# Performance work log

Measured on AMD Instinct MI355X. Metric: run time of the kernel, lower is better.

The kernel has to match this reference:

```python
import jax, jax.numpy as jnp
import numpy as np
from jax import lax

B = 16384; T = 4; DY = 2; H = 64; K = 4; DIM = T * DY
LR = 0.1; EPS_GOAL = 1.0; B1 = 0.9; B2 = 0.999; ADAM_EPS = 1e-8
LOG2PI = float(np.log(2.0 * np.pi))


def setup_inputs() -> dict:
    key = jax.random.key(0)
    ks = jax.random.split(key, 16)
    r = lambda i, shape, s=1.0: jax.random.normal(ks[i], shape, dtype=jnp.float32) * s
    return {
        "visual_features": r(0, (B, 128)),
        "velocity": r(1, (B, 3)),
        "is_at_traffic_light": jax.random.uniform(ks[2], (B, 1), dtype=jnp.float32),
        "traffic_light_state": jax.random.uniform(ks[3], (B, 1), dtype=jnp.float32),
        "goal": r(4, (B, K, DY), 2.0),
        "base_sample": r(5, (DIM,)),
        # merger MLP: 133 -> 64 -> 64 -> 64, ReLU incl. final
        "Wm1": r(6, (133, H), 0.08), "bm1": jnp.zeros((H,), jnp.float32),
        "Wm2": r(7, (H, H), 0.12), "bm2": jnp.zeros((H,), jnp.float32),
        "Wm3": r(8, (H, H), 0.12), "bm3": jnp.zeros((H,), jnp.float32),
        # GRUCell(input=2, hidden=64), torch layout [3H, in], [3H, H]
        "w_ih": r(9, (3 * H, DY), 0.12), "w_hh": r(10, (3 * H, H), 0.12),
        "b_ih": jnp.zeros((3 * H,), jnp.float32), "b_hh": jnp.zeros((3 * H,), jnp.float32),
        # locscale MLP: 64 -> 32 (ReLU) -> 4
        "Wl1": r(11, (H, 32), 0.12), "bl1": jnp.zeros((32,), jnp.float32),
        "Wl2": r(12, (32, 4), 0.12), "bl2": jnp.zeros((4,), jnp.float32),
        "num_steps": 8,
    }


def _gru(x, h, w_ih, w_hh, b_ih, b_hh):
    gi = x @ w_ih.T + b_ih
    gh = h @ w_hh.T + b_hh
    ir, iz, in_ = jnp.split(gi, 3, axis=-1)
    hr, hz, hn = jnp.split(gh, 3, axis=-1)
    r = jax.nn.sigmoid(ir + hr)
    u = jax.nn.sigmoid(iz + hz)
    n = jnp.tanh(in_ + r * hn)
    return (1.0 - u) * n + u * h


def _step_params(y_tm1, z, p):
    w_ih, w_hh, b_ih, b_hh, Wl1, bl1, Wl2, bl2 = p
    z = _gru(y_tm1, z, w_ih, w_hh, b_ih, b_hh)
    ls = jax.nn.relu(z @ Wl1 + bl1) @ Wl2 + bl2  # [B,4]
    dloc = ls[..., :2]
    scale = jax.nn.softplus(ls[..., 2:]) + 0.001
    return z, dloc, scale


def _flow_forward(x, z0, p):
    Bsz = x.shape[0]
    def step(carry, x_t):
        y_tm1, z = carry
        z, dloc, scale = _step_params(y_tm1, z, p)
        y_t = y_tm1 + dloc + scale * x_t
        return (y_t, z), (y_t, scale)
    _, (ys, scales) = lax.scan(step, (jnp.zeros((Bsz, DY), x.dtype), z0), jnp.swapaxes(x, 0, 1))
    y = jnp.swapaxes(ys, 0, 1)        # [B,T,2]
    scales = jnp.swapaxes(scales, 0, 1)
    logabsdet = jnp.sum(jnp.log(jnp.abs(jnp.prod(scales, axis=1))), axis=-1)  # [B]
    return y, logabsdet


def _flow_inverse(y, z0, p):
    Bsz = y.shape[0]
    def step(carry, y_t):
        y_tm1, z = carry
        z, dloc, scale = _step_params(y_tm1, z, p)
        x_t = (y_t - (y_tm1 + dloc)) / scale
        return (y_t, z), (x_t, scale)
    _, (xs, scales) = lax.scan(step, (jnp.zeros((Bsz, DY), y.dtype), z0), jnp.swapaxes(y, 0, 1))
    x = jnp.swapaxes(xs, 0, 1)        # [B,T,2]
    scales = jnp.swapaxes(scales, 0, 1)
    xf = x.reshape(Bsz, -1)
    log_prob = -0.5 * jnp.sum(xf * xf, axis=-1) - 0.5 * DIM * LOG2PI  # std MVN, identity cov
    logabsdet = jnp.sum(jnp.log(jnp.abs(jnp.prod(scales, axis=-1))), axis=-1)  # [B]
    return x, log_prob, logabsdet


def _goal_likelihood(y, goal):
    yl = y[:, -1, :]                               # [B,2]
    d = (yl[:, None, :] - goal) / EPS_GOAL         # [B,K,2]
    comp = -0.5 * jnp.sum(d * d, axis=-1) - DY * (float(np.log(EPS_GOAL)) + 0.5 * LOG2PI)
    lp = jax.nn.logsumexp(comp, axis=-1) - float(np.log(K))
    return jnp.mean(lp)


def _model_forward(visual_features, velocity, is_at_traffic_light, traffic_light_state,
                   goal, base_sample, Wm1, bm1, Wm2, bm2, Wm3, bm3,
                   w_ih, w_hh, b_ih, b_hh, Wl1, bl1, Wl2, bl2, num_steps):
    p = (w_ih, w_hh, b_ih, b_hh, Wl1, bl1, Wl2, bl2)
    feats = jnp.concatenate([visual_features, velocity, is_at_traffic_light, traffic_light_state], axis=-1)
    z = jax.nn.relu(feats @ Wm1 + bm1)
    z = jax.nn.relu(z @ Wm2 + bm2)
    z = jax.nn.relu(z @ Wm3 + bm3)                 # [B,64] contextual params
    Bsz = visual_features.shape[0]
    x0 = jnp.tile(base_sample[None, :], (Bsz, 1)).reshape(Bsz, T, DY)

    def loss_fn(x):
        y, _ = _flow_forward(x, z, p)
        _, log_prob, logabsdet = _flow_inverse(y, z, p)
        imitation_prior = jnp.mean(log_prob - logabsdet)
        return -(imitation_prior + _goal_likelihood(y, goal))

    vg = jax.value_and_grad(loss_fn)

    def adam_step(carry, t):
        x, m, v, xb, lb = carry
        loss, g = vg(x)
        m = B1 * m + (1.0 - B1) * g
        v = B2 * v + (1.0 - B2) * (g * g)
        mh = m / (1.0 - B1 ** t)
        vh = v / (1.0 - B2 ** t)
        xn = x - LR * mh / (jnp.sqrt(vh) + ADAM_EPS)
        better = loss < lb  # torch keeps post-step x when pre-step loss improves
        xb = jnp.where(better, xn, xb)
        lb = jnp.where(better, loss, lb)
        return (xn, m, v, xb, lb), None

    ts = jnp.arange(1, int(num_steps) + 1, dtype=jnp.float32)
    (_, _, _, x_best, _), _ = lax.scan(
        adam_step, (x0, jnp.zeros_like(x0), jnp.zeros_like(x0), x0, jnp.float32(1000.0)), ts)
    y, _ = _flow_forward(x_best, z, p)
    return y


def reference(visual_features, velocity, is_at_traffic_light, traffic_light_state,
              goal, base_sample, Wm1, bm1, Wm2, bm2, Wm3, bm3,
              w_ih, w_hh, b_ih, b_hh, Wl1, bl1, Wl2, bl2, num_steps):
    return _model_forward(visual_features, velocity, is_at_traffic_light, traffic_light_state,
                          goal, base_sample, Wm1, bm1, Wm2, bm2, Wm3, bm3,
                          w_ih, w_hh, b_ih, b_hh, Wl1, bl1, Wl2, bl2, num_steps)
```

## Files before the change

### kernel.cpp

```cpp
#include <hip/hip_runtime.h>
#include <math.h>

#define BATCH 16384
#define NSMAX 8
#define LOG2PI_F 1.8378770664093453f
#define LOG4_F 1.3862943611198906f

typedef _Float16 v8h __attribute__((ext_vector_type(8)));
typedef float    v4f __attribute__((ext_vector_type(4)));
typedef float    v2f __attribute__((ext_vector_type(2)));

#define MFMA16(A,B,C) __builtin_amdgcn_mfma_f32_16x16x32_f16(A,B,C,0,0,0)

__device__ __forceinline__ float bcast(float v, int l) {
    return __uint_as_float(__builtin_amdgcn_readlane(__float_as_uint(v), (unsigned)l));
}
__device__ __forceinline__ float fsigm(float v){ return 1.f/(1.f + __expf(-v)); }
__device__ __forceinline__ float ftanh(float v){ return 1.f - 2.f/(__expf(2.f*v)+1.f); }
__device__ __forceinline__ float fsp(float v){ return fmaxf(v,0.f) + __logf(1.f + __expf(-fabsf(v))); }

__device__ __forceinline__ v8h ld8(const float* p){
    v4f a = *(const v4f*)p; v4f b = *(const v4f*)(p+4);
    v8h r;
    r[0]=(_Float16)a[0]; r[1]=(_Float16)a[1]; r[2]=(_Float16)a[2]; r[3]=(_Float16)a[3];
    r[4]=(_Float16)b[0]; r[5]=(_Float16)b[1]; r[6]=(_Float16)b[2]; r[7]=(_Float16)b[3];
    return r;
}
__device__ __forceinline__ v8h ld8lo(const float* p){
    v4f a = *(const v4f*)p; v4f b = *(const v4f*)(p+4);
    v8h r;
    #pragma unroll
    for (int j=0;j<4;++j){ _Float16 h=(_Float16)a[j]; r[j]=(_Float16)(a[j]-(float)h); }
    #pragma unroll
    for (int j=0;j<4;++j){ _Float16 h=(_Float16)b[j]; r[4+j]=(_Float16)(b[j]-(float)h); }
    return r;
}
__device__ __forceinline__ v8h ld8s(const float* p, int stride){
    v8h r;
    #pragma unroll
    for (int j=0;j<8;++j) r[j] = (_Float16)p[j*stride];
    return r;
}
__device__ __forceinline__ v8h ld8slo(const float* p, int stride){
    v8h r;
    #pragma unroll
    for (int j=0;j<8;++j){ float v=p[j*stride]; _Float16 h=(_Float16)v; r[j]=(_Float16)(v-(float)h); }
    return r;
}
__device__ __forceinline__ unsigned packh2(float a, float b){
    unsigned short au = __builtin_bit_cast(unsigned short, (_Float16)a);
    unsigned short bu = __builtin_bit_cast(unsigned short, (_Float16)b);
    return (unsigned)au | ((unsigned)bu<<16);
}
__device__ __forceinline__ float unpk_lo(unsigned p){
    return (float)__builtin_bit_cast(_Float16,(unsigned short)(p&0xffff));
}
__device__ __forceinline__ float unpk_hi(unsigned p){
    return (float)__builtin_bit_cast(_Float16,(unsigned short)(p>>16));
}

__global__ __launch_bounds__(512) void k_mlp(
    const float* __restrict__ visual, const float* __restrict__ vel,
    const float* __restrict__ tl, const float* __restrict__ tls,
    const float* __restrict__ Wm1, const float* __restrict__ bm1,
    const float* __restrict__ Wm2, const float* __restrict__ bm2,
    const float* __restrict__ Wm3, const float* __restrict__ bm3,
    float* __restrict__ z0ws)
{
    __shared__ float smem[9600];
    const int tid  = threadIdx.x;
    const int lane = tid & 63;
    const int w    = tid >> 6;
    const int b    = blockIdx.x * 8 + w;
    for (int i = tid; i < 8512; i += 512) smem[i] = Wm1[i];
    float* sfeat = smem + 8512 + w * 136;
    sfeat[lane]      = visual[b*128 + lane];
    sfeat[64 + lane] = visual[b*128 + 64 + lane];
    if (lane < 3)  sfeat[128 + lane] = vel[b*3 + lane];
    if (lane == 3) sfeat[131] = tl[b];
    if (lane == 4) sfeat[132] = tls[b];
    __syncthreads();
    float acc = bm1[lane];
    for (int f = 0; f < 133; ++f) acc = fmaf(smem[f*64 + lane], sfeat[f], acc);
    float z1 = fmaxf(acc, 0.f);
    __syncthreads();
    for (int i = tid; i < 4096; i += 512) smem[i] = Wm2[i];
    __syncthreads();
    acc = bm2[lane];
    #pragma unroll 8
    for (int kk = 0; kk < 64; ++kk) acc = fmaf(smem[kk*64 + lane], bcast(z1, kk), acc);
    float z2 = fmaxf(acc, 0.f);
    __syncthreads();
    for (int i = tid; i < 4096; i += 512) smem[i] = Wm3[i];
    __syncthreads();
    acc = bm3[lane];
    #pragma unroll 8
    for (int kk = 0; kk < 64; ++kk) acc = fmaf(smem[kk*64 + lane], bcast(z2, kk), acc);
    z0ws[(size_t)b*64 + lane] = fmaxf(acc, 0.f);
}

__global__ __launch_bounds__(128, 1) void k_adam(
    const float* __restrict__ goal, const float* __restrict__ bs,
    const float* __restrict__ wih, const float* __restrict__ whh,
    const float* __restrict__ bih, const float* __restrict__ bhh,
    const float* __restrict__ Wl1, const float* __restrict__ bl1,
    const float* __restrict__ Wl2, const float* __restrict__ bl2,
    const int*  __restrict__ nsp, const float* __restrict__ z0ws,
    float* __restrict__ traj, float* __restrict__ parts,
    _Float16* __restrict__ ckpt)
{
    __shared__ _Float16 gruLo[12288];
    __shared__ _Float16 whhTf[12288];
    __shared__ _Float16 stageL[2][3200];
    __shared__ float    xsx[2][256];

    const int tid  = threadIdx.x;
    const int w    = tid >> 6;
    const int ln   = tid & 63;
    const int col  = ln & 15;
    const int quad = ln >> 4;
    const int b0   = blockIdx.x*32 + w*16;
    _Float16* sw = stageL[w];
    float*    xw = xsx[w];

    for (int i = tid; i < 24*64; i += 128){
        int f = i>>6, l = i&63, lc = l&15, lq = l>>4;
        int T = f>>1, K = f&1;
        v8h lo = ld8lo(whh + (lc+16*T)*64 + 32*K + lq*8);
        *(v8h*)(gruLo + f*512 + l*8) = lo;
        int Tz = f/6, kc = f - Tz*6;
        v8h th = ld8s(whh + (kc*32+lq*8)*64 + lc + 16*Tz, 64);
        *(v8h*)(whhTf + f*512 + l*8) = th;
    }
    __syncthreads();

    v8h bwh[12][2];
    #pragma unroll
    for (int T=0;T<12;++T){
        int c = col + 16*T;
        bwh[T][0] = ld8(whh + c*64 +      quad*8);
        bwh[T][1] = ld8(whh + c*64 + 32 + quad*8);
    }
    v8h w1h[2][2], w1l[2][2];
    #pragma unroll
    for (int T=0;T<2;++T){
        int n = col + 16*T;
        w1h[T][0] = ld8s  (Wl1 + (     quad*8)*32 + n, 32);
        w1h[T][1] = ld8s  (Wl1 + (32 + quad*8)*32 + n, 32);
        w1l[T][0] = ld8slo(Wl1 + (     quad*8)*32 + n, 32);
        w1l[T][1] = ld8slo(Wl1 + (32 + quad*8)*32 + n, 32);
    }
    v8h awl1[4];
    #pragma unroll
    for (int Tz=0;Tz<4;++Tz)
        awl1[Tz] = ld8(Wl1 + (col+16*Tz)*32 + quad*8);

    float wi0[12], wi1[12];
    #pragma unroll
    for (int T=0;T<12;++T){
        int c = col + 16*T;
        wi0[T] = wih[c*2]; wi1[T] = wih[c*2+1];
    }
    float bsum[8], bn_i[4], bn_h[4];
    #pragma unroll
    for (int T=0;T<8;++T) bsum[T] = bih[col+16*T] + bhh[col+16*T];
    #pragma unroll
    for (int T=0;T<4;++T){
        bn_i[T] = bih[128+col+16*T];
        bn_h[T] = bhh[128+col+16*T];
    }
    float w2[2][4], bl1v[2];
    #pragma unroll
    for (int T=0;T<2;++T){
        int i5 = col + 16*T;
        bl1v[T] = bl1[i5];
        #pragma unroll
        for (int j=0;j<4;++j) w2[T][j] = Wl2[i5*4+j];
    }
    float b2[4] = {bl2[0], bl2[1], bl2[2], bl2[3]};

    float xa0 = bs[2*quad], xa1 = bs[2*quad+1];
    xw[col*16 + 2*quad]   = xa0;
    xw[col*16 + 2*quad+1] = xa1;
    float am0=0,am1=0,av0=0,av1=0,pb1=1.f,pb2=1.f;

    int ns = *nsp; if (ns > NSMAX) ns = NSMAX;

    unsigned rnp[4][4];
    float ug[4][4], ghs[4][4], aa[2][4];
    float s0v[4], s1v[4], c0v[4], c1v[4];
    float zc[4][4];

    auto cell = [&](bool split, const float (&yp0)[4], const float (&yp1)[4],
                    const float (&zprev)[4][4]){
        v8h ah0 = *(const v8h*)(sw + col*200 +      quad*8);
        v8h ah1 = *(const v8h*)(sw + col*200 + 32 + quad*8);
        v8h al0, al1;
        if (split){
            al0 = *(const v8h*)(sw + col*200 + 64 + quad*8);
            al1 = *(const v8h*)(sw + col*200 + 96 + quad*8);
        }
        float znew[4][4];
        #pragma unroll
        for (int Tz=0;Tz<4;++Tz){
            int tr = Tz, tu = Tz+4, tn = Tz+8;
            v8h lr0 = *(const v8h*)(gruLo + (tr*2  )*512 + ln*8);
            v8h lr1 = *(const v8h*)(gruLo + (tr*2+1)*512 + ln*8);
            v8h lu0 = *(const v8h*)(gruLo + (tu*2  )*512 + ln*8);
            v8h lu1 = *(const v8h*)(gruLo + (tu*2+1)*512 + ln*8);
            v8h ln0 = *(const v8h*)(gruLo + (tn*2  )*512 + ln*8);
            v8h ln1 = *(const v8h*)(gruLo + (tn*2+1)*512 + ln*8);
            v4f gr = {0,0,0,0}, gu = {0,0,0,0}, gn = {0,0,0,0};
            gr = MFMA16(ah0, lr0, gr);   gr = MFMA16(ah1, lr1, gr);
            gu = MFMA16(ah0, lu0, gu);   gu = MFMA16(ah1, lu1, gu);
            gn = MFMA16(ah0, ln0, gn);   gn = MFMA16(ah1, ln1, gn);
            if (split){
                gr = MFMA16(al0, bwh[tr][0], gr); gr = MFMA16(al1, bwh[tr][1], gr);
                gu = MFMA16(al0, bwh[tu][0], gu); gu = MFMA16(al1, bwh[tu][1], gu);
                gn = MFMA16(al0, bwh[tn][0], gn); gn = MFMA16(al1, bwh[tn][1], gn);
            }
            gr = MFMA16(ah0, bwh[tr][0], gr); gr = MFMA16(ah1, bwh[tr][1], gr);
            gu = MFMA16(ah0, bwh[tu][0], gu); gu = MFMA16(ah1, bwh[tu][1], gu);
            gn = MFMA16(ah0, bwh[tn][0], gn); gn = MFMA16(ah1, bwh[tn][1], gn);
            #pragma unroll
            for (int r=0;r<4;++r){
                float pr = gr[r] + wi0[Tz]*yp0[r]   + wi1[Tz]*yp1[r]   + bsum[Tz];
                float pu = gu[r] + wi0[Tz+4]*yp0[r] + wi1[Tz+4]*yp1[r] + bsum[Tz+4];
                float gh = gn[r] + bn_h[Tz];
                float gi = wi0[Tz+8]*yp0[r] + wi1[Tz+8]*yp1[r] + bn_i[Tz];
                float R = fsigm(pr), U = fsigm(pu);
                float N = ftanh(gi + R*gh);
                if (!split){ rnp[Tz][r]=packh2(R,N); ug[Tz][r]=U; ghs[Tz][r]=gh; }
                znew[Tz][r] = (1.f-U)*N + U*zprev[Tz][r];
            }
        }
        if (split){
            #pragma unroll
            for (int Tz=0;Tz<4;++Tz)
                #pragma unroll
                for (int r=0;r<4;++r){
                    float v = znew[Tz][r];
                    zc[Tz][r] = v;
                    _Float16 h = (_Float16)v;
                    int o = (quad*4+r)*200 + col + 16*Tz;
                    sw[o] = h; sw[o+64] = (_Float16)(v-(float)h);
                }
        } else {
            #pragma unroll
            for (int Tz=0;Tz<4;++Tz)
                #pragma unroll
                for (int r=0;r<4;++r)
                    sw[(quad*4+r)*200 + col + 16*Tz] = (_Float16)znew[Tz][r];
        }
        v8h bh0 = *(const v8h*)(sw + col*200 +      quad*8);
        v8h bh1 = *(const v8h*)(sw + col*200 + 32 + quad*8);
        v8h bl0, blf;
        if (split){
            bl0 = *(const v8h*)(sw + col*200 + 64 + quad*8);
            blf = *(const v8h*)(sw + col*200 + 96 + quad*8);
        }
        #pragma unroll
        for (int T=0;T<2;++T){
            v4f acc = {0.f,0.f,0.f,0.f};
            acc = MFMA16(bh0, w1l[T][0], acc);
            acc = MFMA16(bh1, w1l[T][1], acc);
            if (split){
                acc = MFMA16(bl0, w1h[T][0], acc);
                acc = MFMA16(blf, w1h[T][1], acc);
            }
            acc = MFMA16(bh0, w1h[T][0], acc);
            acc = MFMA16(bh1, w1h[T][1], acc);
            #pragma unroll
            for (int r=0;r<4;++r) aa[T][r] = fmaxf(acc[r] + bl1v[T], 0.f);
        }
        #pragma unroll
        for (int r=0;r<4;++r){
            float q2 = aa[0][r]*w2[0][2] + aa[1][r]*w2[1][2];
            float q3 = aa[0][r]*w2[0][3] + aa[1][r]*w2[1][3];
            float q0 = 0.f, q1 = 0.f;
            if (split){
                q0 = aa[0][r]*w2[0][0] + aa[1][r]*w2[1][0];
                q1 = aa[0][r]*w2[0][1] + aa[1][r]*w2[1][1];
            }
            #pragma unroll
            for (int m=1;m<16;m<<=1){
                q2 += __shfl_xor(q2,m); q3 += __shfl_xor(q3,m);
                if (split){ q0 += __shfl_xor(q0,m); q1 += __shfl_xor(q1,m); }
            }
            if (split){ c0v[r] = q0 + b2[0]; c1v[r] = q1 + b2[1]; }
            s0v[r] = fsp(q2 + b2[2]) + 0.001f;
            s1v[r] = fsp(q3 + b2[3]) + 0.001f;
        }
    };

    const int crow = ln >> 2;
    const int ccol = (ln & 3) * 16;

    for (int s=0; s<ns; ++s){
        #pragma unroll
        for (int Tz=0;Tz<4;++Tz)
            #pragma unroll
            for (int r=0;r<4;++r){
                float v = z0ws[(size_t)(b0+quad*4+r)*64 + col + 16*Tz];
                zc[Tz][r] = v;
                _Float16 h = (_Float16)v;
                int o = (quad*4+r)*200 + col + 16*Tz;
                sw[o] = h; sw[o+64] = (_Float16)(v-(float)h);
            }
        float y0[4]={0,0,0,0}, y1[4]={0,0,0,0};
        float sumls[4]={0,0,0,0}, sumx2[4]={0,0,0,0};
        #pragma unroll
        for (int t=0;t<4;++t){
            float zprev[4][4];
            #pragma unroll
            for (int Tz=0;Tz<4;++Tz)
                #pragma unroll
                for (int r=0;r<4;++r) zprev[Tz][r] = zc[Tz][r];
            cell(true, y0, y1, zprev);
            #pragma unroll
            for (int r=0;r<4;++r){
                v2f xv = *(const v2f*)(&xw[(quad*4+r)*16 + 2*t]);
                sumx2[r] += xv[0]*xv[0] + xv[1]*xv[1];
                y0[r] += c0v[r] + s0v[r]*xv[0];
                y1[r] += c1v[r] + s1v[r]*xv[1];
                int o = (quad*4+r)*200 + 192 + 2*t;
                sw[o] = (_Float16)y0[r]; sw[o+1] = (_Float16)y1[r];
                sumls[r] += __logf(s0v[r]) + __logf(s1v[r]);
            }
            if (t<3){
                v8h z1 = *(const v8h*)(sw + crow*200 + ccol);
                v8h z2 = *(const v8h*)(sw + crow*200 + ccol + 8);
                _Float16* gp = ckpt + ((size_t)t*BATCH + (b0+crow))*64 + ccol;
                *(v8h*)gp = z1; *(v8h*)(gp+8) = z2;
            }
        }
        float cel[4], yb0[4], yb1[4];
        #pragma unroll
        for (int r=0;r<4;++r){
            const float* gpt = goal + (size_t)(b0+quad*4+r)*8;
            v4f ga = *(const v4f*)gpt; v4f gb = *(const v4f*)(gpt+4);
            float c0_ = -0.5f*((y0[r]-ga[0])*(y0[r]-ga[0]) + (y1[r]-ga[1])*(y1[r]-ga[1])) - LOG2PI_F;
            float c1_ = -0.5f*((y0[r]-ga[2])*(y0[r]-ga[2]) + (y1[r]-ga[3])*(y1[r]-ga[3])) - LOG2PI_F;
            float c2_ = -0.5f*((y0[r]-gb[0])*(y0[r]-gb[0]) + (y1[r]-gb[1])*(y1[r]-gb[1])) - LOG2PI_F;
            float c3_ = -0.5f*((y0[r]-gb[2])*(y0[r]-gb[2]) + (y1[r]-gb[3])*(y1[r]-gb[3])) - LOG2PI_F;
            float mx = fmaxf(fmaxf(c0_,c1_), fmaxf(c2_,c3_));
            float e0 = __expf(c0_-mx), e1 = __expf(c1_-mx), e2 = __expf(c2_-mx), e3 = __expf(c3_-mx);
            float se = e0+e1+e2+e3;
            float lp = mx + __logf(se) - LOG4_F;
            cel[r] = -0.5f*sumx2[r] - 4.f*LOG2PI_F - sumls[r] + lp;
            float inv = 1.f/se;
            yb0[r] = inv*(e0*(ga[0]-y0[r]) + e1*(ga[2]-y0[r]) + e2*(gb[0]-y0[r]) + e3*(gb[2]-y0[r]));
            yb1[r] = inv*(e0*(ga[1]-y1[r]) + e1*(ga[3]-y1[r]) + e2*(gb[1]-y1[r]) + e3*(gb[3]-y1[r]));
        }
        float tsum = cel[0]+cel[1]+cel[2]+cel[3];
        tsum += __shfl_xor(tsum,16); tsum += __shfl_xor(tsum,32);
        if (ln==0) parts[s*1024 + blockIdx.x*2 + w] = tsum;

        float zbN[4][4];
        #pragma unroll
        for (int Tz=0;Tz<4;++Tz){ zbN[Tz][0]=0;zbN[Tz][1]=0;zbN[Tz][2]=0;zbN[Tz][3]=0; }
        #pragma unroll
        for (int tt=0; tt<4; ++tt){
            const int t = 3-tt;
            float zcp[4][4];
            if (t > 0){
                const _Float16* gp = ckpt + ((size_t)(t-1)*BATCH + (b0+crow))*64 + ccol;
                v8h z1 = *(const v8h*)gp; v8h z2 = *(const v8h*)(gp+8);
                *(v8h*)(sw + crow*200 + ccol) = z1;
                *(v8h*)(sw + crow*200 + ccol + 8) = z2;
                #pragma unroll
                for (int Tz=0;Tz<4;++Tz)
                    #pragma unroll
                    for (int r=0;r<4;++r)
                        zcp[Tz][r] = (float)sw[(quad*4+r)*200 + col + 16*Tz];
            } else {
                #pragma unroll
                for (int Tz=0;Tz<4;++Tz)
                    #pragma unroll
                    for (int r=0;r<4;++r){
                        _Float16 h = (_Float16)z0ws[(size_t)(b0+quad*4+r)*64 + col + 16*Tz];
                        zcp[Tz][r] = (float)h;
                        sw[(quad*4+r)*200 + col + 16*Tz] = h;
                    }
            }
            float yp0[4], yp1[4];
            #pragma unroll
            for (int r=0;r<4;++r){
                if (t==0){ yp0[r]=0.f; yp1[r]=0.f; }
                else {
                    int o = (quad*4+r)*200 + 192 + 2*(t-1);
                    yp0[r] = (float)sw[o]; yp1[r] = (float)sw[o+1];
                }
            }
            cell(false, yp0, yp1, zcp);

            float l2[4], l3[4];
            #pragma unroll
            for (int r=0;r<4;++r){
                v2f xv = *(const v2f*)(&xw[(quad*4+r)*16 + 2*t]);
                float sb0 = yb0[r]*xv[0] - 1.f/s0v[r];
                float sb1 = yb1[r]*xv[1] - 1.f/s1v[r];
                float sg0 = 1.f - __expf(-(s0v[r]-0.001f));
                float sg1 = 1.f - __expf(-(s1v[r]-0.001f));
                l2[r] = sb0*sg0; l3[r] = sb1*sg1;
                v2f xb; xb[0] = yb0[r]*s0v[r] - xv[0]; xb[1] = yb1[r]*s1v[r] - xv[1];
                *(v2f*)(&xw[(quad*4+r)*16 + 8 + 2*t]) = xb;
            }
            #pragma unroll
            for (int T=0;T<2;++T)
                #pragma unroll
                for (int r=0;r<4;++r){
                    float ab = w2[T][0]*yb0[r] + w2[T][1]*yb1[r] + w2[T][2]*l2[r] + w2[T][3]*l3[r];
                    ab = (aa[T][r] > 0.f) ? ab : 0.f;
                    sw[(quad*4+r)*200 + 128 + col + 16*T] = (_Float16)ab;
                }
            v8h a_ab = *(const v8h*)(sw + col*200 + 128 + quad*8);
            float dzt[4][4];
            #pragma unroll
            for (int Tz=0;Tz<4;++Tz){
                v4f acc = { zbN[Tz][0], zbN[Tz][1], zbN[Tz][2], zbN[Tz][3] };
                acc = MFMA16(a_ab, awl1[Tz], acc);
                #pragma unroll
                for (int r=0;r<4;++r) dzt[Tz][r] = acc[r];
            }
            float px0[4] = {0,0,0,0}, px1[4] = {0,0,0,0};
            #pragma unroll
            for (int Tz=0;Tz<4;++Tz)
                #pragma unroll
                for (int r=0;r<4;++r){
                    float R = unpk_lo(rnp[Tz][r]);
                    float N = unpk_hi(rnp[Tz][r]);
                    float U = ug[Tz][r], GH = ghs[Tz][r];
                    float nb = dzt[Tz][r]*(1.f-U);
                    float dn = nb*(1.f-N*N);
                    float gnb = dn*R;
                    float rb  = dn*GH;
                    float dr  = rb*R*(1.f-R);
                    float du  = dzt[Tz][r]*(zcp[Tz][r]-N)*U*(1.f-U);
                    int o = (quad*4+r)*200 + col + 16*Tz;
                    sw[o]       = (_Float16)dr;
                    sw[o + 64]  = (_Float16)du;
                    sw[o + 128] = (_Float16)gnb;
                    px0[r] += dr*wi0[Tz] + du*wi0[Tz+4] + dn*wi0[Tz+8];
                    px1[r] += dr*wi1[Tz] + du*wi1[Tz+4] + dn*wi1[Tz+8];
                }
            v8h adg[6];
            #pragma unroll
            for (int kc=0;kc<6;++kc)
                adg[kc] = *(const v8h*)(sw + col*200 + kc*32 + quad*8);
            #pragma unroll
            for (int Tz=0;Tz<4;++Tz){
                v4f acc = { dzt[Tz][0]*ug[Tz][0], dzt[Tz][1]*ug[Tz][1],
                            dzt[Tz][2]*ug[Tz][2], dzt[Tz][3]*ug[Tz][3] };
                #pragma unroll
                for (int kc=0;kc<6;++kc){
                    v8h bwt = *(const v8h*)(whhTf + (Tz*6+kc)*512 + ln*8);
                    acc = MFMA16(adg[kc], bwt, acc);
                }
                #pragma unroll
                for (int r=0;r<4;++r) zbN[Tz][r] = acc[r];
            }
            #pragma unroll
            for (int r=0;r<4;++r){
                float p0 = px0[r], p1 = px1[r];
                #pragma unroll
                for (int m=1;m<16;m<<=1){ p0 += __shfl_xor(p0,m); p1 += __shfl_xor(p1,m); }
                yb0[r] += p0; yb1[r] += p1;
            }
        }
        v2f xb = *(const v2f*)(&xw[col*16 + 8 + 2*quad]);
        float g0 = xb[0] * (-1.f/16384.f), g1 = xb[1] * (-1.f/16384.f);
        am0 = 0.9f*am0 + 0.1f*g0;        am1 = 0.9f*am1 + 0.1f*g1;
        av0 = 0.999f*av0 + 0.001f*g0*g0; av1 = 0.999f*av1 + 0.001f*g1*g1;
        pb1 *= 0.9f; pb2 *= 0.999f;
        float ic1 = 1.f/(1.f-pb1), ic2 = 1.f/(1.f-pb2);
        xa0 -= 0.1f*(am0*ic1)/(sqrtf(av0*ic2) + 1e-8f);
        xa1 -= 0.1f*(am1*ic1)/(sqrtf(av1*ic2) + 1e-8f);
        xw[col*16 + 2*quad]   = xa0;
        xw[col*16 + 2*quad+1] = xa1;
        v2f tv; tv[0]=xa0; tv[1]=xa1;
        *(v2f*)(traj + (size_t)(b0+col)*64 + s*8 + 2*quad) = tv;
    }
}

__global__ void k_pick(const int* __restrict__ nsp,
                       const float* __restrict__ parts, int* __restrict__ best)
{
    int ln = threadIdx.x & 63;
    int ns = *nsp; if (ns > NSMAX) ns = NSMAX;
    float losses[NSMAX];
    for (int s=0;s<NSMAX;++s){
        float acc = 0.f;
        if (s < ns){
            for (int i=ln;i<1024;i+=64) acc += parts[s*1024+i];
            #pragma unroll
            for (int m=1;m<64;m<<=1) acc += __shfl_xor(acc,m);
        }
        losses[s] = -acc * (1.f/16384.f);
    }
    if (ln==0 && blockIdx.x==0){
        float lb = 1000.f; int bi = -1;
        for (int s=0;s<ns;++s) if (losses[s] < lb){ lb = losses[s]; bi = s; }
        best[0] = bi;
    }
}

__global__ __launch_bounds__(128, 1) void k_final(
    const float* __restrict__ bs,
    const float* __restrict__ wih, const float* __restrict__ whh,
    const float* __restrict__ bih, const float* __restrict__ bhh,
    const float* __restrict__ Wl1, const float* __restrict__ bl1,
    const float* __restrict__ Wl2, const float* __restrict__ bl2,
    const float* __restrict__ z0ws, const float* __restrict__ traj,
    const int* __restrict__ best, float* __restrict__ outp)
{
    __shared__ _Float16 gruLo[12288];
    __shared__ _Float16 stageL[2][3200];
    __shared__ float    xsx[2][128];

    const int tid  = threadIdx.x;
    const int w    = tid >> 6;
    const int ln   = tid & 63;
    const int col  = ln & 15;
    const int quad = ln >> 4;
    const int b0   = blockIdx.x*32 + w*16;
    _Float16* sw = stageL[w];
    float*    xw = xsx[w];

    for (int i = tid; i < 24*64; i += 128){
        int f = i>>6, l = i&63, lc = l&15, lq = l>>4;
        int T = f>>1, K = f&1;
        v8h lo = ld8lo(whh + (lc+16*T)*64 + 32*K + lq*8);
        *(v8h*)(gruLo + f*512 + l*8) = lo;
    }
    __syncthreads();

    v8h bwh[12][2];
    #pragma unroll
    for (int T=0;T<12;++T){
        int c = col + 16*T;
        bwh[T][0] = ld8(whh + c*64 +      quad*8);
        bwh[T][1] = ld8(whh + c*64 + 32 + quad*8);
    }
    v8h w1h[2][2], w1l[2][2];
    #pragma unroll
    for (int T=0;T<2;++T){
        int n = col + 16*T;
        w1h[T][0] = ld8s  (Wl1 + (     quad*8)*32 + n, 32);
        w1h[T][1] = ld8s  (Wl1 + (32 + quad*8)*32 + n, 32);
        w1l[T][0] = ld8slo(Wl1 + (     quad*8)*32 + n, 32);
        w1l[T][1] = ld8slo(Wl1 + (32 + quad*8)*32 + n, 32);
    }
    float wi0[12], wi1[12], bsum[8], bn_i[4], bn_h[4];
    #pragma unroll
    for (int T=0;T<12;++T){
        int c = col + 16*T;
        wi0[T] = wih[c*2]; wi1[T] = wih[c*2+1];
    }
    #pragma unroll
    for (int T=0;T<8;++T) bsum[T] = bih[col+16*T] + bhh[col+16*T];
    #pragma unroll
    for (int T=0;T<4;++T){
        bn_i[T] = bih[128+col+16*T];
        bn_h[T] = bhh[128+col+16*T];
    }
    float w2[2][4], bl1v[2];
    #pragma unroll
    for (int T=0;T<2;++T){
        int i5 = col + 16*T;
        bl1v[T] = bl1[i5];
        #pragma unroll
        for (int j=0;j<4;++j) w2[T][j] = Wl2[i5*4+j];
    }
    float b2[4] = {bl2[0], bl2[1], bl2[2], bl2[3]};

    float zc[4][4];
    #pragma unroll
    for (int Tz=0;Tz<4;++Tz)
        #pragma unroll
        for (int r=0;r<4;++r){
            float v = z0ws[(size_t)(b0+quad*4+r)*64 + col + 16*Tz];
            zc[Tz][r] = v;
            _Float16 h = (_Float16)v;
            int o = (quad*4+r)*200 + col + 16*Tz;
            sw[o] = h; sw[o+64] = (_Float16)(v-(float)h);
        }

    int bi = best[0];
    float x0i, x1i;
    if (bi >= 0){
        v2f xv = *(const v2f*)(traj + (size_t)(b0+col)*64 + bi*8 + 2*quad);
        x0i = xv[0]; x1i = xv[1];
    } else { x0i = bs[2*quad]; x1i = bs[2*quad+1]; }
    xw[col*8 + 2*quad]   = x0i;
    xw[col*8 + 2*quad+1] = x1i;

    float y0[4]={0,0,0,0}, y1[4]={0,0,0,0};
    #pragma unroll
    for (int t=0;t<4;++t){
        v8h ah0 = *(const v8h*)(sw + col*200 +      quad*8);
        v8h ah1 = *(const v8h*)(sw + col*200 + 32 + quad*8);
        v8h al0 = *(const v8h*)(sw + col*200 + 64 + quad*8);
        v8h al1 = *(const v8h*)(sw + col*200 + 96 + quad*8);
        #pragma unroll
        for (int Tz=0;Tz<4;++Tz){
            int tr = Tz, tu = Tz+4, tn = Tz+8;
            v8h lr0 = *(const v8h*)(gruLo + (tr*2  )*512 + ln*8);
            v8h lr1 = *(const v8h*)(gruLo + (tr*2+1)*512 + ln*8);
            v8h lu0 = *(const v8h*)(gruLo + (tu*2  )*512 + ln*8);
            v8h lu1 = *(const v8h*)(gruLo + (tu*2+1)*512 + ln*8);
            v8h ln0 = *(const v8h*)(gruLo + (tn*2  )*512 + ln*8);
            v8h ln1 = *(const v8h*)(gruLo + (tn*2+1)*512 + ln*8);
            v4f gr = {0,0,0,0}, gu = {0,0,0,0}, gn = {0,0,0,0};
            gr = MFMA16(ah0, lr0, gr);   gr = MFMA16(ah1, lr1, gr);
            gu = MFMA16(ah0, lu0, gu);   gu = MFMA16(ah1, lu1, gu);
            gn = MFMA16(ah0, ln0, gn);   gn = MFMA16(ah1, ln1, gn);
            gr = MFMA16(al0, bwh[tr][0], gr); gr = MFMA16(al1, bwh[tr][1], gr);
            gu = MFMA16(al0, bwh[tu][0], gu); gu = MFMA16(al1, bwh[tu][1], gu);
            gn = MFMA16(al0, bwh[tn][0], gn); gn = MFMA16(al1, bwh[tn][1], gn);
            gr = MFMA16(ah0, bwh[tr][0], gr); gr = MFMA16(ah1, bwh[tr][1], gr);
            gu = MFMA16(ah0, bwh[tu][0], gu); gu = MFMA16(ah1, bwh[tu][1], gu);
            gn = MFMA16(ah0, bwh[tn][0], gn); gn = MFMA16(ah1, bwh[tn][1], gn);
            #pragma unroll
            for (int r=0;r<4;++r){
                float pr = gr[r] + wi0[Tz]*y0[r]   + wi1[Tz]*y1[r]   + bsum[Tz];
                float pu = gu[r] + wi0[Tz+4]*y0[r] + wi1[Tz+4]*y1[r] + bsum[Tz+4];
                float gh = gn[r] + bn_h[Tz];
                float gi = wi0[Tz+8]*y0[r] + wi1[Tz+8]*y1[r] + bn_i[Tz];
                float R = fsigm(pr), U = fsigm(pu);
                float N = ftanh(gi + R*gh);
                zc[Tz][r] = (1.f-U)*N + U*zc[Tz][r];
            }
        }
        #pragma unroll
        for (int Tz=0;Tz<4;++Tz)
            #pragma unroll
            for (int r=0;r<4;++r){
                float v = zc[Tz][r];
                _Float16 h = (_Float16)v;
                int o = (quad*4+r)*200 + col + 16*Tz;
                sw[o] = h; sw[o+64] = (_Float16)(v-(float)h);
            }
        v8h bh0 = *(const v8h*)(sw + col*200 +      quad*8);
        v8h bh1 = *(const v8h*)(sw + col*200 + 32 + quad*8);
        v8h bl0 = *(const v8h*)(sw + col*200 + 64 + quad*8);
        v8h blf = *(const v8h*)(sw + col*200 + 96 + quad*8);
        float aaf[2][4];
        #pragma unroll
        for (int T=0;T<2;++T){
            v4f acc = {0.f,0.f,0.f,0.f};
            acc = MFMA16(bh0, w1l[T][0], acc);
            acc = MFMA16(bh1, w1l[T][1], acc);
            acc = MFMA16(bl0, w1h[T][0], acc);
            acc = MFMA16(blf, w1h[T][1], acc);
            acc = MFMA16(bh0, w1h[T][0], acc);
            acc = MFMA16(bh1, w1h[T][1], acc);
            #pragma unroll
            for (int r=0;r<4;++r) aaf[T][r] = fmaxf(acc[r] + bl1v[T], 0.f);
        }
        #pragma unroll
        for (int r=0;r<4;++r){
            float q0 = aaf[0][r]*w2[0][0] + aaf[1][r]*w2[1][0];
            float q1 = aaf[0][r]*w2[0][1] + aaf[1][r]*w2[1][1];
            float q2 = aaf[0][r]*w2[0][2] + aaf[1][r]*w2[1][2];
            float q3 = aaf[0][r]*w2[0][3] + aaf[1][r]*w2[1][3];
            #pragma unroll
            for (int m=1;m<16;m<<=1){
                q0 += __shfl_xor(q0,m); q1 += __shfl_xor(q1,m);
                q2 += __shfl_xor(q2,m); q3 += __shfl_xor(q3,m);
            }
            float c0 = q0 + b2[0], c1 = q1 + b2[1];
            float s0 = fsp(q2 + b2[2]) + 0.001f;
            float s1 = fsp(q3 + b2[3]) + 0.001f;
            float xv0 = xw[(quad*4+r)*8 + 2*t];
            float xv1 = xw[(quad*4+r)*8 + 2*t + 1];
            y0[r] += c0 + s0*xv0;
            y1[r] += c1 + s1*xv1;
            if (col == 0){
                v2f o; o[0]=y0[r]; o[1]=y1[r];
                *(v2f*)(outp + (size_t)(b0+quad*4+r)*8 + 2*t) = o;
            }
        }
    }
}

extern "C" void kernel_launch(void* const* d_in, const int* in_sizes, int n_in,
                              void* d_out, int out_size, void* d_ws, size_t ws_size,
                              hipStream_t stream)
{
    const float* visual = (const float*)d_in[0];
    const float* vel    = (const float*)d_in[1];
    const float* tl     = (const float*)d_in[2];
    const float* tls    = (const float*)d_in[3];
    const float* goal   = (const float*)d_in[4];
    const float* bs     = (const float*)d_in[5];
    const float* Wm1    = (const float*)d_in[6];
    const float* bm1    = (const float*)d_in[7];
    const float* Wm2    = (const float*)d_in[8];
    const float* bm2    = (const float*)d_in[9];
    const float* Wm3    = (const float*)d_in[10];
    const float* bm3    = (const float*)d_in[11];
    const float* wih    = (const float*)d_in[12];
    const float* whh    = (const float*)d_in[13];
    const float* bih    = (const float*)d_in[14];
    const float* bhh    = (const float*)d_in[15];
    const float* Wl1    = (const float*)d_in[16];
    const float* bl1    = (const float*)d_in[17];
    const float* Wl2    = (const float*)d_in[18];
    const float* bl2    = (const float*)d_in[19];
    const int*   nsp    = (const int*)d_in[20];

    float* z0ws  = (float*)d_ws;
    float* traj  = z0ws + (size_t)BATCH * 64;
    float* parts = traj + (size_t)BATCH * 64;
    int*   best  = (int*)(parts + NSMAX*1024);
    _Float16* ckpt = (_Float16*)(best + 4);

    k_mlp<<<BATCH/8, 512, 0, stream>>>(visual, vel, tl, tls,
        Wm1, bm1, Wm2, bm2, Wm3, bm3, z0ws);

    k_adam<<<BATCH/32, 128, 0, stream>>>(goal, bs,
        wih, whh, bih, bhh, Wl1, bl1, Wl2, bl2,
        nsp, z0ws, traj, parts, ckpt);

    k_pick<<<1, 64, 0, stream>>>(nsp, parts, best);

    k_final<<<BATCH/32, 128, 0, stream>>>(bs,
        wih, whh, bih, bhh, Wl1, bl1, Wl2, bl2,
        z0ws, traj, best, (float*)d_out);
}
```

Measured before the change: 813.5 us.

## Move GRU hidden weights from registers to LDS and time-share one LDS buffer

The high-half W_hh fragments (bwh, 48 v8h registers per lane) are no longer held in registers and are instead read from a new LDS buffer gruHi in both the Adam and final kernels. In the Adam kernel, the low-half and transposed weight buffers share one LDS region (regB), which is refilled from global memory twice per optimization step with added __syncthreads barriers. The aim is to cut register pressure and LDS footprint, at the cost of extra LDS reads, per-step global reloads and block barriers. MFMA accumulation order is also regrouped per gate.

```diff
diff --git a/kernel.cpp b/kernel.cpp
--- a/kernel.cpp
+++ b/kernel.cpp
@@ -109,8 +109,8 @@
     float* __restrict__ traj, float* __restrict__ parts,
     _Float16* __restrict__ ckpt)
 {
-    __shared__ _Float16 gruLo[12288];
-    __shared__ _Float16 whhTf[12288];
+    __shared__ _Float16 gruHi[12288];
+    __shared__ _Float16 regB [12288];
     __shared__ _Float16 stageL[2][3200];
     __shared__ float    xsx[2][256];
 
@@ -123,24 +123,29 @@
     _Float16* sw = stageL[w];
     float*    xw = xsx[w];
 
-    for (int i = tid; i < 24*64; i += 128){
-        int f = i>>6, l = i&63, lc = l&15, lq = l>>4;
-        int T = f>>1, K = f&1;
-        v8h lo = ld8lo(whh + (lc+16*T)*64 + 32*K + lq*8);
-        *(v8h*)(gruLo + f*512 + l*8) = lo;
-        int Tz = f/6, kc = f - Tz*6;
-        v8h th = ld8s(whh + (kc*32+lq*8)*64 + lc + 16*Tz, 64);
-        *(v8h*)(whhTf + f*512 + l*8) = th;
-    }
-    __syncthreads();
-
-    v8h bwh[12][2];
-    #pragma unroll
-    for (int T=0;T<12;++T){
-        int c = col + 16*T;
-        bwh[T][0] = ld8(whh + c*64 +      quad*8);
-        bwh[T][1] = ld8(whh + c*64 + 32 + quad*8);
-    }
+    auto fillHi = [&](){
+        for (int i = tid; i < 24*64; i += 128){
+            int f = i>>6, l = i&63, lc = l&15, lq = l>>4;
+            int T = f>>1, K = f&1;
+            *(v8h*)(gruHi + f*512 + l*8) = ld8(whh + (lc+16*T)*64 + 32*K + lq*8);
+        }
+    };
+    auto fillLo = [&](){
+        for (int i = tid; i < 24*64; i += 128){
+            int f = i>>6, l = i&63, lc = l&15, lq = l>>4;
+            int T = f>>1, K = f&1;
+            *(v8h*)(regB + f*512 + l*8) = ld8lo(whh + (lc+16*T)*64 + 32*K + lq*8);
+        }
+    };
+    auto fillT = [&](){
+        for (int i = tid; i < 24*64; i += 128){
+            int f = i>>6, l = i&63, lc = l&15, lq = l>>4;
+            int Tz = f/6, kc = f - Tz*6;
+            *(v8h*)(regB + f*512 + l*8) = ld8s(whh + (kc*32+lq*8)*64 + lc + 16*Tz, 64);
+        }
+    };
+    fillHi();
+
     v8h w1h[2][2], w1l[2][2];
     #pragma unroll
     for (int T=0;T<2;++T){
@@ -203,30 +208,30 @@
         float znew[4][4];
         #pragma unroll
         for (int Tz=0;Tz<4;++Tz){
-            int tr = Tz, tu = Tz+4, tn = Tz+8;
-            v8h lr0 = *(const v8h*)(gruLo + (tr*2  )*512 + ln*8);
-            v8h lr1 = *(const v8h*)(gruLo + (tr*2+1)*512 + ln*8);
-            v8h lu0 = *(const v8h*)(gruLo + (tu*2  )*512 + ln*8);
-            v8h lu1 = *(const v8h*)(gruLo + (tu*2+1)*512 + ln*8);
-            v8h ln0 = *(const v8h*)(gruLo + (tn*2  )*512 + ln*8);
-            v8h ln1 = *(const v8h*)(gruLo + (tn*2+1)*512 + ln*8);
-            v4f gr = {0,0,0,0}, gu = {0,0,0,0}, gn = {0,0,0,0};
-            gr = MFMA16(ah0, lr0, gr);   gr = MFMA16(ah1, lr1, gr);
-            gu = MFMA16(ah0, lu0, gu);   gu = MFMA16(ah1, lu1, gu);
-            gn = MFMA16(ah0, ln0, gn);   gn = MFMA16(ah1, ln1, gn);
-            if (split){
-                gr = MFMA16(al0, bwh[tr][0], gr); gr = MFMA16(al1, bwh[tr][1], gr);
-                gu = MFMA16(al0, bwh[tu][0], gu); gu = MFMA16(al1, bwh[tu][1], gu);
-                gn = MFMA16(al0, bwh[tn][0], gn); gn = MFMA16(al1, bwh[tn][1], gn);
-            }
-            gr = MFMA16(ah0, bwh[tr][0], gr); gr = MFMA16(ah1, bwh[tr][1], gr);
-            gu = MFMA16(ah0, bwh[tu][0], gu); gu = MFMA16(ah1, bwh[tu][1], gu);
-            gn = MFMA16(ah0, bwh[tn][0], gn); gn = MFMA16(ah1, bwh[tn][1], gn);
+            v4f g3[3];
+            #pragma unroll
+            for (int gg=0; gg<3; ++gg){
+                int tg = Tz + 4*gg;
+                v8h h0 = *(const v8h*)(gruHi + (tg*2  )*512 + ln*8);
+                v8h h1 = *(const v8h*)(gruHi + (tg*2+1)*512 + ln*8);
+                v4f acc = {0,0,0,0};
+                if (split){
+                    v8h l0 = *(const v8h*)(regB + (tg*2  )*512 + ln*8);
+                    v8h l1 = *(const v8h*)(regB + (tg*2+1)*512 + ln*8);
+                    acc = MFMA16(ah0, l0, acc);
+                    acc = MFMA16(ah1, l1, acc);
+                    acc = MFMA16(al0, h0, acc);
+                    acc = MFMA16(al1, h1, acc);
+                }
+                acc = MFMA16(ah0, h0, acc);
+                acc = MFMA16(ah1, h1, acc);
+                g3[gg] = acc;
+            }
             #pragma unroll
             for (int r=0;r<4;++r){
-                float pr = gr[r] + wi0[Tz]*yp0[r]   + wi1[Tz]*yp1[r]   + bsum[Tz];
-                float pu = gu[r] + wi0[Tz+4]*yp0[r] + wi1[Tz+4]*yp1[r] + bsum[Tz+4];
-                float gh = gn[r] + bn_h[Tz];
+                float pr = g3[0][r] + wi0[Tz]*yp0[r]   + wi1[Tz]*yp1[r]   + bsum[Tz];
+                float pu = g3[1][r] + wi0[Tz+4]*yp0[r] + wi1[Tz+4]*yp1[r] + bsum[Tz+4];
+                float gh = g3[2][r] + bn_h[Tz];
                 float gi = wi0[Tz+8]*yp0[r] + wi1[Tz+8]*yp1[r] + bn_i[Tz];
                 float R = fsigm(pr), U = fsigm(pu);
                 float N = ftanh(gi + R*gh);
@@ -297,6 +302,9 @@
     const int ccol = (ln & 3) * 16;
 
     for (int s=0; s<ns; ++s){
+        __syncthreads();
+        fillLo();
+        __syncthreads();
         #pragma unroll
         for (int Tz=0;Tz<4;++Tz)
             #pragma unroll
@@ -355,6 +363,10 @@
         float tsum = cel[0]+cel[1]+cel[2]+cel[3];
         tsum += __shfl_xor(tsum,16); tsum += __shfl_xor(tsum,32);
         if (ln==0) parts[s*1024 + blockIdx.x*2 + w] = tsum;
+
+        __syncthreads();
+        fillT();
+        __syncthreads();
 
         float zbN[4][4];
         #pragma unroll
@@ -454,7 +466,7 @@
                             dzt[Tz][2]*ug[Tz][2], dzt[Tz][3]*ug[Tz][3] };
                 #pragma unroll
                 for (int kc=0;kc<6;++kc){
-                    v8h bwt = *(const v8h*)(whhTf + (Tz*6+kc)*512 + ln*8);
+                    v8h bwt = *(const v8h*)(regB + (Tz*6+kc)*512 + ln*8);
                     acc = MFMA16(adg[kc], bwt, acc);
                 }
                 #pragma unroll
@@ -514,6 +526,7 @@
     const float* __restrict__ z0ws, const float* __restrict__ traj,
     const int* __restrict__ best, float* __restrict__ outp)
 {
+    __shared__ _Float16 gruHi[12288];
     __shared__ _Float16 gruLo[12288];
     __shared__ _Float16 stageL[2][3200];
     __shared__ float    xsx[2][128];
@@ -530,18 +543,11 @@
     for (int i = tid; i < 24*64; i += 128){
         int f = i>>6, l = i&63, lc = l&15, lq = l>>4;
         int T = f>>1, K = f&1;
-        v8h lo = ld8lo(whh + (lc+16*T)*64 + 32*K + lq*8);
-        *(v8h*)(gruLo + f*512 + l*8) = lo;
+        *(v8h*)(gruHi + f*512 + l*8) = ld8  (whh + (lc+16*T)*64 + 32*K + lq*8);
+        *(v8h*)(gruLo + f*512 + l*8) = ld8lo(whh + (lc+16*T)*64 + 32*K + lq*8);
     }
     __syncthreads();
 
-    v8h bwh[12][2];
-    #pragma unroll
-    for (int T=0;T<12;++T){
-        int c = col + 16*T;
-        bwh[T][0] = ld8(whh + c*64 +      quad*8);
-        bwh[T][1] = ld8(whh + c*64 + 32 + quad*8);
-    }
     v8h w1h[2][2], w1l[2][2];
     #pragma unroll
     for (int T=0;T<2;++T){
@@ -604,28 +610,28 @@
         v8h al1 = *(const v8h*)(sw + col*200 + 96 + quad*8);
         #pragma unroll
         for (int Tz=0;Tz<4;++Tz){
-            int tr = Tz, tu = Tz+4, tn = Tz+8;
-            v8h lr0 = *(const v8h*)(gruLo + (tr*2  )*512 + ln*8);
-            v8h lr1 = *(const v8h*)(gruLo + (tr*2+1)*512 + ln*8);
-            v8h lu0 = *(const v8h*)(gruLo + (tu*2  )*512 + ln*8);
-            v8h lu1 = *(const v8h*)(gruLo + (tu*2+1)*512 + ln*8);
-            v8h ln0 = *(const v8h*)(gruLo + (tn*2  )*512 + ln*8);
-            v8h ln1 = *(const v8h*)(gruLo + (tn*2+1)*512 + ln*8);
-            v4f gr = {0,0,0,0}, gu = {0,0,0,0}, gn = {0,0,0,0};
-            gr = MFMA16(ah0, lr0, gr);   gr = MFMA16(ah1, lr1, gr);
-            gu = MFMA16(ah0, lu0, gu);   gu = MFMA16(ah1, lu1, gu);
-            gn = MFMA16(ah0, ln0, gn);   gn = MFMA16(ah1, ln1, gn);
-            gr = MFMA16(al0, bwh[tr][0], gr); gr = MFMA16(al1, bwh[tr][1], gr);
-            gu = MFMA16(al0, bwh[tu][0], gu); gu = MFMA16(al1, bwh[tu][1], gu);
-            gn = MFMA16(al0, bwh[tn][0], gn); gn = MFMA16(al1, bwh[tn][1], gn);
-            gr = MFMA16(ah0, bwh[tr][0], gr); gr = MFMA16(ah1, bwh[tr][1], gr);
-            gu = MFMA16(ah0, bwh[tu][0], gu); gu = MFMA16(ah1, bwh[tu][1], gu);
-            gn = MFMA16(ah0, bwh[tn][0], gn); gn = MFMA16(ah1, bwh[tn][1], gn);
+            v4f g3[3];
+            #pragma unroll
+            for (int gg=0; gg<3; ++gg){
+                int tg = Tz + 4*gg;
+                v8h h0 = *(const v8h*)(gruHi + (tg*2  )*512 + ln*8);
+                v8h h1 = *(const v8h*)(gruHi + (tg*2+1)*512 + ln*8);
+                v8h l0 = *(const v8h*)(gruLo + (tg*2  )*512 + ln*8);
+                v8h l1 = *(const v8h*)(gruLo + (tg*2+1)*512 + ln*8);
+                v4f acc = {0,0,0,0};
+                acc = MFMA16(ah0, l0, acc);
+                acc = MFMA16(ah1, l1, acc);
+                acc = MFMA16(al0, h0, acc);
+                acc = MFMA16(al1, h1, acc);
+                acc = MFMA16(ah0, h0, acc);
+                acc = MFMA16(ah1, h1, acc);
+                g3[gg] = acc;
+            }
             #pragma unroll
             for (int r=0;r<4;++r){
-                float pr = gr[r] + wi0[Tz]*y0[r]   + wi1[Tz]*y1[r]   + bsum[Tz];
-                float pu = gu[r] + wi0[Tz+4]*y0[r] + wi1[Tz+4]*y1[r] + bsum[Tz+4];
-                float gh = gn[r] + bn_h[Tz];
+                float pr = g3[0][r] + wi0[Tz]*y0[r]   + wi1[Tz]*y1[r]   + bsum[Tz];
+                float pu = g3[1][r] + wi0[Tz+4]*y0[r] + wi1[Tz+4]*y1[r] + bsum[Tz+4];
+                float gh = g3[2][r] + bn_h[Tz];
                 float gi = wi0[Tz+8]*y0[r] + wi1[Tz+8]*y1[r] + bn_i[Tz];
                 float R = fsigm(pr), U = fsigm(pu);
                 float N = ftanh(gi + R*gh);
```

Result: slower. 1.836 ms (+125.7%).
